# Kernel optimization log

Hardware: AMD Instinct MI355X
Metric: run time of the kernel (lower is better)

## Reference

```python
import jax, jax.numpy as jnp
import numpy as np

B, S, D, H, F = 2, 2048, 1024, 16, 4096
DK = D // H
EPS = 1e-6


def _ln(x, g, b):
    mu = jnp.mean(x, axis=-1, keepdims=True)
    var = jnp.mean(jnp.square(x - mu), axis=-1, keepdims=True)
    return (x - mu) * jax.lax.rsqrt(var + EPS) * g + b


def setup_inputs() -> dict:
    key = jax.random.key(0)
    ks = jax.random.split(key, 8)
    sc = 0.02
    return {
        "x": jax.random.normal(ks[0], (B, S, D), jnp.float32),
        "wq": jax.random.normal(ks[1], (D, D), jnp.float32) * sc,
        "bq": jnp.zeros((D,), jnp.float32),
        "wk": jax.random.normal(ks[2], (D, D), jnp.float32) * sc,
        "bk": jnp.zeros((D,), jnp.float32),
        "wv": jax.random.normal(ks[3], (D, D), jnp.float32) * sc,
        "bv": jnp.zeros((D,), jnp.float32),
        "wo": jax.random.normal(ks[4], (D, D), jnp.float32) * sc,
        "bo": jnp.zeros((D,), jnp.float32),
        "w1": jax.random.normal(ks[5], (D, F), jnp.float32) * sc,
        "b1": jnp.zeros((F,), jnp.float32),
        "w2": jax.random.normal(ks[6], (F, D), jnp.float32) * sc,
        "b2": jnp.zeros((D,), jnp.float32),
        "g1": jnp.ones((D,), jnp.float32),
        "be1": jnp.zeros((D,), jnp.float32),
        "g2": jnp.ones((D,), jnp.float32),
        "be2": jnp.zeros((D,), jnp.float32),
    }


def reference(x, wq, bq, wk, bk, wv, bv, wo, bo, w1, b1, w2, b2, g1, be1, g2, be2):
    # Multi-head self-attention (no masks, eval-mode dropout = identity)
    q = (x @ wq + bq).reshape(B, S, H, DK)
    k = (x @ wk + bk).reshape(B, S, H, DK)
    v = (x @ wv + bv).reshape(B, S, H, DK)
    scale = 1.0 / (DK ** 0.5)
    score = jnp.einsum('bihd,bjhd->bhij', q, k) * scale  # [B,H,S,S]
    p = jax.nn.softmax(score, axis=-1)
    attn = jnp.einsum('bhij,bjhd->bihd', p, v).reshape(B, S, D)
    attn = attn @ wo + bo
    # residual + LayerNorm 1
    h = _ln(x + attn, g1, be1)
    # FFN (relu) + residual + LayerNorm 2
    ff = jax.nn.relu(h @ w1 + b1) @ w2 + b2
    return _ln(h + ff, g2, be2)
```

## Files before the change

kernel.cpp:

```cpp
#include <hip/hip_runtime.h>
#include <hip/hip_bf16.h>
#include <cmath>

typedef __bf16 bf16_t;
typedef __bf16 bf16x4 __attribute__((ext_vector_type(4)));
typedef __bf16 bf16x8 __attribute__((ext_vector_type(8)));
typedef float  f32x4  __attribute__((ext_vector_type(4)));

__device__ __forceinline__ void gld_lds16(const bf16_t* g, bf16_t* l) {
    __builtin_amdgcn_global_load_lds(
        (const __attribute__((address_space(1))) void*)g,
        (__attribute__((address_space(3))) void*)l,
        16, 0, 0);
}

struct PrepArgs {
    const float* w[6]; bf16_t* wt[6];
    int K[6], N[6], start[6];
    const float* x; bf16_t* xb; int castStart;
    const float* bq; const float* bk; float* bqkv; int biasStart;
};

__global__ __launch_bounds__(256) void prep(PrepArgs pa) {
    __shared__ float tile[32][33];
    const int bid = blockIdx.x, t = threadIdx.x;
    if (bid < pa.castStart) {
        int mi = 0;
#pragma unroll
        for (int i = 1; i < 6; i++) if (bid >= pa.start[i]) mi = i;
        const int tt  = bid - pa.start[mi];
        const int nbx = pa.N[mi] >> 5;
        const int n0 = (tt % nbx) * 32, k0 = (tt / nbx) * 32;
        const float* in = pa.w[mi];
        bf16_t* out = pa.wt[mi];
        const int K = pa.K[mi], N = pa.N[mi];
        const int tx = t & 31, ty = t >> 5;
#pragma unroll
        for (int i = 0; i < 4; i++) {
            int kk = ty + i * 8;
            tile[kk][tx] = in[(size_t)(k0 + kk) * N + n0 + tx];
        }
        __syncthreads();
#pragma unroll
        for (int i = 0; i < 4; i++) {
            int nn = ty + i * 8;
            out[(size_t)(n0 + nn) * K + k0 + tx] = (bf16_t)tile[tx][nn];
        }
    } else if (bid < pa.biasStart) {
        int i = (bid - pa.castStart) * 256 + t;
        f32x4 v = ((const f32x4*)pa.x)[i];
        bf16x4 o;
        o[0] = (bf16_t)v[0]; o[1] = (bf16_t)v[1]; o[2] = (bf16_t)v[2]; o[3] = (bf16_t)v[3];
        ((bf16x4*)pa.xb)[i] = o;
    } else {
#pragma unroll
        for (int j = 0; j < 8; j++) {
            int idx = t * 8 + j;
            pa.bqkv[idx] = idx < 1024 ? pa.bq[idx] : pa.bk[idx - 1024];
        }
    }
}

template<int MT>
__global__ __launch_bounds__(256) void gemm_bt(
    const bf16_t* __restrict__ A, const bf16_t* __restrict__ Bt,
    const float* __restrict__ bias,
    float* __restrict__ Cf, bf16_t* __restrict__ Cb,
    int M, int N, int lda, int Kloc, int relu, int nbn, int bias_row,
    long bt_bstride, long c_bstride) {
    constexpr int TM = MT * 32;
    __shared__ __attribute__((aligned(16))) bf16_t As[2][TM * 32];
    __shared__ __attribute__((aligned(16))) bf16_t Bs[2][128 * 32];
    const int tid  = threadIdx.x;
    const int lane = tid & 63;
    const int wave = tid >> 6;
    const int wm = wave & 1, wn = wave >> 1;
    const int kh = blockIdx.z;

    const int span  = 8 * nbn;
    const int group = blockIdx.x / span;
    const int rem   = blockIdx.x % span;
    const int bm    = group * 8 + (rem & 7);
    const int bn    = rem >> 3;

    const bf16_t* Bt_b = Bt + (size_t)blockIdx.y * bt_bstride;
    float*  Cf_b = Cf ? Cf + (size_t)blockIdx.y * c_bstride + (size_t)kh * M * N : nullptr;
    bf16_t* Cb_b = Cb ? Cb + (size_t)blockIdx.y * c_bstride : nullptr;
    const int koff = kh * Kloc;

    const int r4 = tid >> 2;
    const int kc = (tid & 3) * 8;
    const bf16_t* Ag = A    + (size_t)(bm * TM  + r4) * lda + koff + kc;
    const bf16_t* Bg = Bt_b + (size_t)(bn * 128 + r4) * lda + koff + kc;

    f32x4 acc[MT][4] = {};
    const int mrow = lane & 15;
    const int q8   = (lane >> 4) * 8;

    auto stage = [&](int kk, int buf) {
#pragma unroll
        for (int i = 0; i < MT / 2; i++)
            gld_lds16(Ag + (size_t)(i * 64) * lda + kk, &As[buf][i * 64 * 32] + tid * 8);
        gld_lds16(Bg + kk,                        &Bs[buf][0] + tid * 8);
        gld_lds16(Bg + (size_t)64 * lda + kk,     &Bs[buf][64 * 32] + tid * 8);
    };

    stage(0, 0);
    __syncthreads();

    const int nt = Kloc >> 5;
    for (int t7 = 0; t7 < nt; ++t7) {
        const int cur = t7 & 1;
        if (t7 + 1 < nt) stage((t7 + 1) << 5, cur ^ 1);

        bf16x8 af[MT], bfr[4];
#pragma unroll
        for (int mt = 0; mt < MT; mt++)
            af[mt] = *(const bf16x8*)(&As[cur][(wm * (MT * 16) + mt * 16 + mrow) * 32 + q8]);
#pragma unroll
        for (int nt2 = 0; nt2 < 4; nt2++)
            bfr[nt2] = *(const bf16x8*)(&Bs[cur][(wn * 64 + nt2 * 16 + mrow) * 32 + q8]);
#pragma unroll
        for (int mt = 0; mt < MT; mt++)
#pragma unroll
            for (int nt2 = 0; nt2 < 4; nt2++)
                acc[mt][nt2] = __builtin_amdgcn_mfma_f32_16x16x32_bf16(
                    af[mt], bfr[nt2], acc[mt][nt2], 0, 0, 0);

        __syncthreads();
    }

    const int rq = (lane >> 4) * 4;
#pragma unroll
    for (int mt = 0; mt < MT; mt++) {
        int row0 = bm * TM + wm * (MT * 16) + mt * 16 + rq;
#pragma unroll
        for (int nt2 = 0; nt2 < 4; nt2++) {
            int col = bn * 128 + wn * 64 + nt2 * 16 + mrow;
            float bvc = (bias && kh == 0 && !bias_row) ? bias[col] : 0.f;
#pragma unroll
            for (int r = 0; r < 4; r++) {
                float bb = (bias && kh == 0 && bias_row) ? bias[row0 + r] : bvc;
                float v = acc[mt][nt2][r] + bb;
                if (relu) v = fmaxf(v, 0.f);
                size_t idx = (size_t)(row0 + r) * N + col;
                if (Cf_b) Cf_b[idx] = v;
                if (Cb_b) Cb_b[idx] = (bf16_t)v;
            }
        }
    }
}

__global__ __launch_bounds__(256) void flash_attn_mfma(
    const bf16_t* __restrict__ QKb,
    const bf16_t* __restrict__ Vtg,
    bf16_t* __restrict__ Outb) {
    __shared__ __attribute__((aligned(16))) bf16_t Ks[2][4096];
    __shared__ __attribute__((aligned(16))) bf16_t Vs[2][4096];
    __shared__ __attribute__((aligned(16))) bf16_t Ps[4096];
    const int t = threadIdx.x;
    const int lane = t & 63, wave = t >> 6;
    const int g = lane >> 4, cl = lane & 15;
    const int b = blockIdx.z, h = blockIdx.y, q0 = blockIdx.x * 64;
    const int RS = 2048;
    const bf16_t* Qg = QKb + (size_t)(b * 2048 + q0) * RS + h * 64;
    const bf16_t* Kg = QKb + (size_t)(b * 2048) * RS + 1024 + h * 64;
    const bf16_t* Vg = Vtg + ((size_t)b * 1024 + h * 64) * 2048;

    const int sr = t >> 2;
    const int sc = (t & 3) * 8;

    const bf16_t* Qrow = Qg + (size_t)(wave * 16 + cl) * RS;
    bf16x8 qr0 = *(const bf16x8*)(Qrow + g * 8);
    bf16x8 qr1 = *(const bf16x8*)(Qrow + 32 + g * 8);

    gld_lds16(Kg + (size_t)sr * RS + sc,        &Ks[0][0]    + t * 8);
    gld_lds16(Kg + (size_t)sr * RS + 32 + sc,   &Ks[0][2048] + t * 8);
    gld_lds16(Vg + (size_t)sr * 2048 + sc,      &Vs[0][0]    + t * 8);
    gld_lds16(Vg + (size_t)sr * 2048 + 32 + sc, &Vs[0][2048] + t * 8);
    __syncthreads();

    f32x4 Oacc[4] = {};
    f32x4 Lacc = {};
    bf16x8 ones;
#pragma unroll
    for (int j = 0; j < 8; j++) ones[j] = (bf16_t)1.0f;

    const int rowb = wave * 16 + cl;
    const int psw  = (cl & 7) << 4;
    char* PsB = (char*)Ps;
    const float C = 0.125f * 1.4426950408889634f;

    for (int kt_i = 0; kt_i < 32; ++kt_i) {
        const int cur = kt_i & 1;
        if (kt_i + 1 < 32) {
            const int nb  = cur ^ 1;
            const int ktn = (kt_i + 1) * 64;
            gld_lds16(Kg + (size_t)(ktn + sr) * RS + sc,        &Ks[nb][0]    + t * 8);
            gld_lds16(Kg + (size_t)(ktn + sr) * RS + 32 + sc,   &Ks[nb][2048] + t * 8);
            gld_lds16(Vg + (size_t)sr * 2048 + ktn + sc,        &Vs[nb][0]    + t * 8);
            gld_lds16(Vg + (size_t)sr * 2048 + ktn + 32 + sc,   &Vs[nb][2048] + t * 8);
        }

        f32x4 Sacc[4] = {};
        __builtin_amdgcn_s_setprio(1);
#pragma unroll
        for (int ks = 0; ks < 2; ++ks) {
            bf16x8 bq = ks ? qr1 : qr0;
#pragma unroll
            for (int mt = 0; mt < 4; ++mt) {
                bf16x8 ak = *(const bf16x8*)(&Ks[cur][ks * 2048 + (mt * 16 + cl) * 32 + g * 8]);
                Sacc[mt] = __builtin_amdgcn_mfma_f32_16x16x32_bf16(ak, bq, Sacc[mt], 0, 0, 0);
            }
        }
        __builtin_amdgcn_s_setprio(0);

#pragma unroll
        for (int mt = 0; mt < 4; ++mt) {
            bf16x4 p4;
#pragma unroll
            for (int r = 0; r < 4; r++)
                p4[r] = (bf16_t)__builtin_amdgcn_exp2f(Sacc[mt][r] * C);
            *(bf16x4*)(PsB + ((rowb * 128 + mt * 32 + g * 8) ^ psw)) = p4;
        }

        __builtin_amdgcn_s_setprio(1);
#pragma unroll
        for (int ks = 0; ks < 2; ++ks) {
            bf16x8 ap = *(const bf16x8*)(PsB + ((rowb * 128 + ks * 64 + g * 16) ^ psw));
            Lacc = __builtin_amdgcn_mfma_f32_16x16x32_bf16(ap, ones, Lacc, 0, 0, 0);
#pragma unroll
            for (int nt = 0; nt < 4; ++nt) {
                bf16x8 bv = *(const bf16x8*)(&Vs[cur][ks * 2048 + (nt * 16 + cl) * 32 + g * 8]);
                Oacc[nt] = __builtin_amdgcn_mfma_f32_16x16x32_bf16(ap, bv, Oacc[nt], 0, 0, 0);
            }
        }
        __builtin_amdgcn_s_setprio(0);

        __syncthreads();
    }

#pragma unroll
    for (int r = 0; r < 4; r++) {
        float inv = 1.f / Lacc[r];
        int qrow = q0 + wave * 16 + g * 4 + r;
        size_t base = (size_t)(b * 2048 + qrow) * 1024 + h * 64;
#pragma unroll
        for (int nt = 0; nt < 4; nt++)
            Outb[base + nt * 16 + cl] = (bf16_t)(Oacc[nt][r] * inv);
    }
}

__global__ __launch_bounds__(256) void resid_ln3(const float* __restrict__ a,
                                                 const float* __restrict__ p0,
                                                 const float* __restrict__ p1,
                                                 const float* __restrict__ g,
                                                 const float* __restrict__ be,
                                                 float* __restrict__ outf,
                                                 bf16_t* __restrict__ outb) {
    const int row = blockIdx.x, t = threadIdx.x;
    const size_t base = (size_t)row * 1024;
    f32x4 v = ((const f32x4*)(a + base))[t] + ((const f32x4*)(p0 + base))[t];
    if (p1) v += ((const f32x4*)(p1 + base))[t];
    float sum = v[0] + v[1] + v[2] + v[3];
    float sq  = v[0] * v[0] + v[1] * v[1] + v[2] * v[2] + v[3] * v[3];
#pragma unroll
    for (int o = 1; o < 64; o <<= 1) {
        sum += __shfl_xor(sum, o);
        sq  += __shfl_xor(sq, o);
    }
    __shared__ float red[8];
    int wave = t >> 6, lane = t & 63;
    if (lane == 0) { red[wave] = sum; red[4 + wave] = sq; }
    __syncthreads();
    sum = red[0] + red[1] + red[2] + red[3];
    sq  = red[4] + red[5] + red[6] + red[7];
    float mu  = sum * (1.f / 1024.f);
    float var = sq * (1.f / 1024.f) - mu * mu;
    float rs  = rsqrtf(var + 1e-6f);
    f32x4 g4 = ((const f32x4*)g)[t];
    f32x4 b4 = ((const f32x4*)be)[t];
    f32x4 o = (v - mu) * rs * g4 + b4;
    ((f32x4*)(outf + base))[t] = o;
    if (outb) {
        bf16x4 ob;
        ob[0] = (bf16_t)o[0]; ob[1] = (bf16_t)o[1]; ob[2] = (bf16_t)o[2]; ob[3] = (bf16_t)o[3];
        ((bf16x4*)(outb + base))[t] = ob;
    }
}

extern "C" void kernel_launch(void* const* d_in, const int* in_sizes, int n_in,
                              void* d_out, int out_size, void* d_ws, size_t ws_size,
                              hipStream_t stream) {
    (void)in_sizes; (void)n_in; (void)out_size; (void)ws_size;
    const float* x   = (const float*)d_in[0];
    const float* wq  = (const float*)d_in[1];
    const float* bq  = (const float*)d_in[2];
    const float* wk  = (const float*)d_in[3];
    const float* bk  = (const float*)d_in[4];
    const float* wv  = (const float*)d_in[5];
    const float* bv  = (const float*)d_in[6];
    const float* wo  = (const float*)d_in[7];
    const float* bo  = (const float*)d_in[8];
    const float* w1  = (const float*)d_in[9];
    const float* b1  = (const float*)d_in[10];
    const float* w2  = (const float*)d_in[11];
    const float* b2  = (const float*)d_in[12];
    const float* g1  = (const float*)d_in[13];
    const float* be1 = (const float*)d_in[14];
    const float* g2  = (const float*)d_in[15];
    const float* be2 = (const float*)d_in[16];
    float* out = (float*)d_out;

    char* ws = (char*)d_ws;
    const size_t MB = 1ull << 20;
    bf16_t* xb    = (bf16_t*)(ws + 0);
    bf16_t* WtQKV = (bf16_t*)(ws + 8 * MB);
    bf16_t* WtO   = (bf16_t*)(ws + 14 * MB);
    bf16_t* Wt1   = (bf16_t*)(ws + 16 * MB);
    bf16_t* Wt2   = (bf16_t*)(ws + 24 * MB);
    float*  bqkv  = (float*)(ws + 32 * MB);
    bf16_t* QKb   = (bf16_t*)(ws + 33 * MB);
    bf16_t* Vt    = (bf16_t*)(ws + 49 * MB);
    bf16_t* ffb   = (bf16_t*)(ws + 33 * MB);
    float*  oa    = (float*)(ws + 65 * MB);
    float*  f2    = (float*)(ws + 65 * MB);
    float*  hbuf  = (float*)(ws + 97 * MB);
    bf16_t* hb    = (bf16_t*)(ws + 113 * MB);
    bf16_t* ab    = xb;
    const int MN = 4096 * 1024;

    PrepArgs pa;
    pa.w[0] = wq; pa.w[1] = wk; pa.w[2] = wv; pa.w[3] = wo; pa.w[4] = w1; pa.w[5] = w2;
    pa.wt[0] = WtQKV; pa.wt[1] = WtQKV + 1024 * 1024; pa.wt[2] = WtQKV + 2048 * 1024;
    pa.wt[3] = WtO; pa.wt[4] = Wt1; pa.wt[5] = Wt2;
    int Ks[6] = {1024, 1024, 1024, 1024, 1024, 4096};
    int Ns[6] = {1024, 1024, 1024, 1024, 4096, 1024};
    int st[6] = {0, 1024, 2048, 3072, 4096, 8192};
    for (int i = 0; i < 6; i++) { pa.K[i] = Ks[i]; pa.N[i] = Ns[i]; pa.start[i] = st[i]; }
    pa.x = x; pa.xb = xb; pa.castStart = 12288;
    pa.bq = bq; pa.bk = bk; pa.bqkv = bqkv; pa.biasStart = 12288 + 4096;
    prep<<<12288 + 4096 + 1, 256, 0, stream>>>(pa);

    gemm_bt<4><<<512, 256, 0, stream>>>(xb, WtQKV, bqkv, nullptr, QKb,
                                        4096, 2048, 1024, 1024, 0, 16, 0, 0, 0);
    gemm_bt<2><<<dim3(256, 2, 1), 256, 0, stream>>>(WtQKV + 2048 * 1024, xb, bv,
                                        nullptr, Vt, 1024, 2048, 1024, 1024, 0, 16, 1,
                                        (long)2048 * 1024, (long)1024 * 2048);
    flash_attn_mfma<<<dim3(32, 16, 2), 256, 0, stream>>>(QKb, Vt, ab);
    gemm_bt<4><<<dim3(256, 1, 2), 256, 0, stream>>>(ab, WtO, bo, oa, nullptr,
                                        4096, 1024, 1024, 512, 0, 8, 0, 0, 0);
    resid_ln3<<<4096, 256, 0, stream>>>(x, oa, oa + MN, g1, be1, hbuf, hb);
    gemm_bt<4><<<1024, 256, 0, stream>>>(hb, Wt1, b1, nullptr, ffb,
                                         4096, 4096, 1024, 1024, 1, 32, 0, 0, 0);
    gemm_bt<4><<<dim3(256, 1, 2), 256, 0, stream>>>(ffb, Wt2, b2, f2, nullptr,
                                        4096, 1024, 4096, 2048, 0, 8, 0, 0, 0);
    resid_ln3<<<4096, 256, 0, stream>>>(hbuf, f2, f2 + MN, g2, be2, out, nullptr);
}
```

Measured before the change: 419.4 us.

## Add 256-row tile GEMM with 512 threads for projection and FFN GEMMs

Adds a new bf16 MFMA GEMM kernel using 256xBN output tiles, 8 waves per block and K steps of 64 split into two 32-wide LDS halves with double buffering. It replaces the old 128-row tile GEMM for the QK projection, output projection and both FFN GEMMs. Larger tiles raise arithmetic intensity and cut global and LDS reloads, but the per-thread accumulator arrays grow a lot (up to 8x4 f32x4), which risks register spills and lower occupancy. Grid sizes shrink, so fewer blocks are available to fill the CUs.

Result: faster. 397.9 us (-5.1%).

```diff
diff --git a/kernel.cpp b/kernel.cpp
--- a/kernel.cpp
+++ b/kernel.cpp
@@ -57,6 +57,107 @@
         for (int j = 0; j < 8; j++) {
             int idx = t * 8 + j;
             pa.bqkv[idx] = idx < 1024 ? pa.bq[idx] : pa.bk[idx - 1024];
+        }
+    }
+}
+
+template<int BN>
+__global__ __launch_bounds__(512, 2) void gemm_bt256(
+    const bf16_t* __restrict__ A, const bf16_t* __restrict__ Bt,
+    const float* __restrict__ bias,
+    float* __restrict__ Cf, bf16_t* __restrict__ Cb,
+    int M, int N, int lda, int Kloc, int relu, int nbn,
+    long bt_bstride, long c_bstride) {
+    constexpr int NT = BN / 64;
+    constexpr int WN = BN / 4;
+    __shared__ __attribute__((aligned(16))) bf16_t As[2][2][256 * 32];
+    __shared__ __attribute__((aligned(16))) bf16_t Bs[2][2][BN * 32];
+    const int tid  = threadIdx.x;
+    const int lane = tid & 63;
+    const int wave = tid >> 6;
+    const int wm = wave >> 2, wn = wave & 3;
+    const int kh = blockIdx.z;
+
+    const int span  = 8 * nbn;
+    const int group = blockIdx.x / span;
+    const int rem   = blockIdx.x % span;
+    const int bm    = group * 8 + (rem & 7);
+    const int bn    = rem >> 3;
+
+    const bf16_t* Bt_b = Bt + (size_t)blockIdx.y * bt_bstride;
+    float*  Cf_b = Cf ? Cf + (size_t)blockIdx.y * c_bstride + (size_t)kh * M * N : nullptr;
+    bf16_t* Cb_b = Cb ? Cb + (size_t)blockIdx.y * c_bstride : nullptr;
+    const int koff = kh * Kloc;
+
+    const int r4 = tid >> 2;
+    const int kc = (tid & 3) * 8;
+    const bf16_t* Ag = A    + (size_t)(bm * 256 + r4) * lda + koff + kc;
+    const bf16_t* Bg = Bt_b + (size_t)(bn * BN  + r4) * lda + koff + kc;
+
+    f32x4 acc[8][NT] = {};
+    const int mrow = lane & 15;
+    const int q8   = (lane >> 4) * 8;
+
+    auto stage = [&](int kk, int buf) {
+#pragma unroll
+        for (int hh = 0; hh < 2; hh++) {
+#pragma unroll
+            for (int i = 0; i < 2; i++)
+                gld_lds16(Ag + (size_t)(i * 128) * lda + kk + hh * 32,
+                          &As[buf][hh][i * 128 * 32] + tid * 8);
+            if (BN == 256) {
+#pragma unroll
+                for (int i = 0; i < 2; i++)
+                    gld_lds16(Bg + (size_t)(i * 128) * lda + kk + hh * 32,
+                              &Bs[buf][hh][i * 128 * 32] + tid * 8);
+            } else {
+                gld_lds16(Bg + kk + hh * 32, &Bs[buf][hh][0] + tid * 8);
+            }
+        }
+    };
+
+    stage(0, 0);
+    __syncthreads();
+
+    const int nsteps = Kloc >> 6;
+    for (int st = 0; st < nsteps; ++st) {
+        const int cur = st & 1;
+        if (st + 1 < nsteps) stage((st + 1) << 6, cur ^ 1);
+
+#pragma unroll
+        for (int hh = 0; hh < 2; hh++) {
+            bf16x8 bfr[NT];
+#pragma unroll
+            for (int n = 0; n < NT; n++)
+                bfr[n] = *(const bf16x8*)(&Bs[cur][hh][(wn * WN + n * 16 + mrow) * 32 + q8]);
+#pragma unroll
+            for (int mt = 0; mt < 8; mt++) {
+                bf16x8 af = *(const bf16x8*)(&As[cur][hh][(wm * 128 + mt * 16 + mrow) * 32 + q8]);
+#pragma unroll
+                for (int n = 0; n < NT; n++)
+                    acc[mt][n] = __builtin_amdgcn_mfma_f32_16x16x32_bf16(
+                        af, bfr[n], acc[mt][n], 0, 0, 0);
+            }
+        }
+        __syncthreads();
+    }
+
+    const int rq = (lane >> 4) * 4;
+#pragma unroll
+    for (int mt = 0; mt < 8; mt++) {
+        int row0 = bm * 256 + wm * 128 + mt * 16 + rq;
+#pragma unroll
+        for (int n = 0; n < NT; n++) {
+            int col = bn * BN + wn * WN + n * 16 + mrow;
+            float bvc = (bias && kh == 0) ? bias[col] : 0.f;
+#pragma unroll
+            for (int r = 0; r < 4; r++) {
+                float v = acc[mt][n][r] + bvc;
+                if (relu) v = fmaxf(v, 0.f);
+                size_t idx = (size_t)(row0 + r) * N + col;
+                if (Cf_b) Cf_b[idx] = v;
+                if (Cb_b) Cb_b[idx] = (bf16_t)v;
+            }
         }
     }
 }
@@ -342,18 +443,18 @@
     pa.bq = bq; pa.bk = bk; pa.bqkv = bqkv; pa.biasStart = 12288 + 4096;
     prep<<<12288 + 4096 + 1, 256, 0, stream>>>(pa);
 
-    gemm_bt<4><<<512, 256, 0, stream>>>(xb, WtQKV, bqkv, nullptr, QKb,
-                                        4096, 2048, 1024, 1024, 0, 16, 0, 0, 0);
+    gemm_bt256<128><<<256, 512, 0, stream>>>(xb, WtQKV, bqkv, nullptr, QKb,
+                                        4096, 2048, 1024, 1024, 0, 16, 0, 0);
     gemm_bt<2><<<dim3(256, 2, 1), 256, 0, stream>>>(WtQKV + 2048 * 1024, xb, bv,
                                         nullptr, Vt, 1024, 2048, 1024, 1024, 0, 16, 1,
                                         (long)2048 * 1024, (long)1024 * 2048);
     flash_attn_mfma<<<dim3(32, 16, 2), 256, 0, stream>>>(QKb, Vt, ab);
-    gemm_bt<4><<<dim3(256, 1, 2), 256, 0, stream>>>(ab, WtO, bo, oa, nullptr,
-                                        4096, 1024, 1024, 512, 0, 8, 0, 0, 0);
+    gemm_bt256<128><<<dim3(128, 1, 2), 512, 0, stream>>>(ab, WtO, bo, oa, nullptr,
+                                        4096, 1024, 1024, 512, 0, 8, 0, 0);
     resid_ln3<<<4096, 256, 0, stream>>>(x, oa, oa + MN, g1, be1, hbuf, hb);
-    gemm_bt<4><<<1024, 256, 0, stream>>>(hb, Wt1, b1, nullptr, ffb,
-                                         4096, 4096, 1024, 1024, 1, 32, 0, 0, 0);
-    gemm_bt<4><<<dim3(256, 1, 2), 256, 0, stream>>>(ffb, Wt2, b2, f2, nullptr,
-                                        4096, 1024, 4096, 2048, 0, 8, 0, 0, 0);
+    gemm_bt256<256><<<256, 512, 0, stream>>>(hb, Wt1, b1, nullptr, ffb,
+                                         4096, 4096, 1024, 1024, 1, 16, 0, 0);
+    gemm_bt256<128><<<dim3(128, 1, 2), 512, 0, stream>>>(ffb, Wt2, b2, f2, nullptr,
+                                        4096, 1024, 4096, 2048, 0, 8, 0, 0);
     resid_ln3<<<4096, 256, 0, stream>>>(hbuf, f2, f2 + MN, g2, be2, out, nullptr);
 }
```
